# Kernel tuning notes

Measured on AMD Instinct MI355X. Metric: run time of the kernel, lower is better.

## Reference

```python
import jax, jax.numpy as jnp
import numpy as np

N_NODES = 100000
N_EDGES = 1600000
IN_DIM, HID_DIM, OUT_DIM = 256, 128, 64


def gcn_conv(x, row, col, w, W, b, n):
    # PyG GCNConv (eval): add self-loops (weight 1), symmetric normalization,
    # linear transform, scatter-add aggregation at target nodes.
    row = jnp.concatenate([row, jnp.arange(n, dtype=row.dtype)])
    col = jnp.concatenate([col, jnp.arange(n, dtype=col.dtype)])
    w = jnp.concatenate([w, jnp.ones((n,), dtype=w.dtype)])
    deg = jax.ops.segment_sum(w, col, num_segments=n)  # [N]
    dinv = jnp.where(deg > 0, jax.lax.rsqrt(deg), 0.0)
    norm = dinv[row] * w * dinv[col]  # [E+N]
    h = x @ W  # [N, out]
    msg = norm[:, None] * h[row]  # gather: [E+N, out]
    out = jax.ops.segment_sum(msg, col, num_segments=n)  # scatter-add
    return out + b


def setup_inputs() -> dict:
    key = jax.random.key(0)
    k = jax.random.split(key, 8)
    x = jax.random.normal(k[0], (N_NODES, IN_DIM), dtype=jnp.float32)
    edge_index = jax.random.randint(k[1], (2, N_EDGES), 0, N_NODES, dtype=jnp.int64)
    edge_weight = jax.random.uniform(k[2], (N_EDGES,), dtype=jnp.float32)
    s1 = 1.0 / np.sqrt(IN_DIM)
    s2 = 1.0 / np.sqrt(HID_DIM)
    W1 = jax.random.uniform(k[3], (IN_DIM, HID_DIM), minval=-s1, maxval=s1, dtype=jnp.float32)
    b1 = jnp.zeros((HID_DIM,), dtype=jnp.float32)
    W2 = jax.random.uniform(k[4], (HID_DIM, OUT_DIM), minval=-s2, maxval=s2, dtype=jnp.float32)
    b2 = jnp.zeros((OUT_DIM,), dtype=jnp.float32)
    return {"x": x, "edge_index": edge_index, "edge_weight": edge_weight,
            "W1": W1, "b1": b1, "W2": W2, "b2": b2}


def reference(x, edge_index, edge_weight, W1, b1, W2, b2):
    row, col = edge_index[0], edge_index[1]
    n = x.shape[0]
    h = gcn_conv(x, row, col, edge_weight, W1, b1, n)
    h = jax.nn.relu(h)  # dropout is identity in eval mode
    out = gcn_conv(h, row, col, edge_weight, W2, b2, n)
    return out
```

## Files before the change

### kernel.cpp

```cpp
#include <hip/hip_runtime.h>
#include <hip/hip_fp16.h>

#define IN_DIM 256
#define HID_DIM 128
#define OUT_DIM 64

typedef short s8v __attribute__((ext_vector_type(8)));
typedef float f32x4 __attribute__((ext_vector_type(4)));


__device__ __forceinline__ unsigned short bf16_rne(float f) {
    unsigned int u = __float_as_uint(f);
    u += 0x7FFFu + ((u >> 16) & 1u);
    return (unsigned short)(u >> 16);
}
__device__ __forceinline__ float bfbits_to_f(unsigned short h) {
    return __uint_as_float(((unsigned int)h) << 16);
}
__device__ __forceinline__ void cvt_split4(float4 f, uint2& hv, uint2& lv) {
    unsigned short h0 = bf16_rne(f.x), h1 = bf16_rne(f.y);
    unsigned short h2 = bf16_rne(f.z), h3 = bf16_rne(f.w);
    unsigned short l0 = bf16_rne(f.x - bfbits_to_f(h0));
    unsigned short l1 = bf16_rne(f.y - bfbits_to_f(h1));
    unsigned short l2 = bf16_rne(f.z - bfbits_to_f(h2));
    unsigned short l3 = bf16_rne(f.w - bfbits_to_f(h3));
    hv.x = (unsigned int)h0 | ((unsigned int)h1 << 16);
    hv.y = (unsigned int)h2 | ((unsigned int)h3 << 16);
    lv.x = (unsigned int)l0 | ((unsigned int)l1 << 16);
    lv.y = (unsigned int)l2 | ((unsigned int)l3 << 16);
}

__global__ __launch_bounds__(256) void wsplit_kernel(const float* __restrict__ W,
        unsigned short* __restrict__ wth, unsigned short* __restrict__ wtl,
        int K, int NCOL) {
    int idx = blockIdx.x * 256 + threadIdx.x;
    if (idx < K * NCOL) {
        int k = idx / NCOL, nn = idx % NCOL;
        float f = W[idx];
        unsigned short h = bf16_rne(f);
        unsigned short l = bf16_rne(f - bfbits_to_f(h));
        wth[nn * K + k] = h;
        wtl[nn * K + k] = l;
    }
}


#define FPSCALE 16777216.0f
#define FPMASK  ((1ULL << 40) - 1)

__global__ __launch_bounds__(256) void init_kernel(unsigned long long* packed, int n) {
    int i = blockIdx.x * 256 + threadIdx.x;
    if (i < n) packed[i] = (1ULL << 24);
}

__global__ __launch_bounds__(256) void deg_cnt_kernel(const int* __restrict__ col,
        const float* __restrict__ w, unsigned long long* packed,
        int* __restrict__ arr, int e) {
    int i = blockIdx.x * 256 + threadIdx.x;
    if (i < e) {
        unsigned long long v = (1ULL << 40) |
            (unsigned long long)(w[i] * FPSCALE + 0.5f);
        unsigned long long old = atomicAdd(&packed[col[i]], v);
        arr[i] = (int)(old >> 40);
    }
}

__global__ __launch_bounds__(256) void dinv_kernel(const unsigned long long* __restrict__ packed,
        float* __restrict__ dinv, int* __restrict__ cnt, int n) {
    int i = blockIdx.x * 256 + threadIdx.x;
    if (i < n) {
        unsigned long long p = packed[i];
        float d = (float)(p & FPMASK) * (1.0f / FPSCALE);
        dinv[i] = d > 0.0f ? rsqrtf(d) : 0.0f;
        cnt[i] = (int)(p >> 40);
    }
}


__global__ __launch_bounds__(256) void scan1_kernel(const int* __restrict__ cnt,
        int* __restrict__ bsum, int n) {
    int t = threadIdx.x;
    int base = blockIdx.x * 1024 + t * 4;
    int s = 0;
    if (base + 3 < n) {
        int4 v = *(const int4*)(cnt + base);
        s = v.x + v.y + v.z + v.w;
    } else {
        for (int i = 0; i < 4; i++) if (base + i < n) s += cnt[base + i];
    }
    __shared__ int sm[256];
    sm[t] = s;
    __syncthreads();
    for (int d = 1; d < 256; d <<= 1) {
        int v = (t >= d) ? sm[t - d] : 0;
        __syncthreads();
        sm[t] += v;
        __syncthreads();
    }
    if (t == 255) bsum[blockIdx.x] = sm[255];
}

__global__ __launch_bounds__(1024) void scan2_kernel(int* bsum, int* total_out, int nb) {
    __shared__ int sm[1024];
    int t = threadIdx.x;
    int v = (t < nb) ? bsum[t] : 0;
    sm[t] = v;
    __syncthreads();
    for (int d = 1; d < 1024; d <<= 1) {
        int u = (t >= d) ? sm[t - d] : 0;
        __syncthreads();
        sm[t] += u;
        __syncthreads();
    }
    int ex = (t == 0) ? 0 : sm[t - 1];
    if (t < nb) bsum[t] = ex;
    if (t == nb - 1) *total_out = sm[t];
}

__global__ __launch_bounds__(256) void scan3_kernel(const int* __restrict__ cnt,
        const int* __restrict__ bsum, int* __restrict__ offsets, int n) {
    int t = threadIdx.x;
    int base = blockIdx.x * 1024 + t * 4;
    int a[4] = {0, 0, 0, 0};
    if (base + 3 < n) {
        int4 v = *(const int4*)(cnt + base);
        a[0] = v.x; a[1] = v.y; a[2] = v.z; a[3] = v.w;
    } else {
        for (int i = 0; i < 4; i++) if (base + i < n) a[i] = cnt[base + i];
    }
    int s = a[0] + a[1] + a[2] + a[3];
    __shared__ int sm[256];
    sm[t] = s;
    __syncthreads();
    for (int d = 1; d < 256; d <<= 1) {
        int u = (t >= d) ? sm[t - d] : 0;
        __syncthreads();
        sm[t] += u;
        __syncthreads();
    }
    int pre = bsum[blockIdx.x] + ((t == 0) ? 0 : sm[t - 1]);
    int o0 = pre, o1 = o0 + a[0], o2 = o1 + a[1], o3 = o2 + a[2];
    if (base + 3 < n) {
        *(int4*)(offsets + base) = make_int4(o0, o1, o2, o3);
    } else {
        int o[4] = {o0, o1, o2, o3};
        for (int i = 0; i < 4; i++) if (base + i < n) offsets[base + i] = o[i];
    }
}


__global__ __launch_bounds__(256) void fill_csc_kernel(const int* __restrict__ row,
        const int* __restrict__ col, const float* __restrict__ w,
        const int* __restrict__ offsets, const int* __restrict__ arr,
        int2* __restrict__ csc, int e) {
    int i = blockIdx.x * 256 + threadIdx.x;
    if (i < e) {
        int c = col[i];
        int p = offsets[c] + arr[i];
        csc[p] = make_int2(row[i], __float_as_int(w[i]));
    }
}


template<int K, int NCOL>
__global__ __launch_bounds__(256) void gemm_mfma_kernel(
        const float* __restrict__ x, const unsigned short* __restrict__ wth,
        const unsigned short* __restrict__ wtl, const float* __restrict__ dinv,
        __half* __restrict__ out, int n) {
    constexpr int NT = NCOL / 16;
    constexpr int NCH = K / 32;
    __shared__ unsigned short sAh[128 * 40];
    __shared__ unsigned short sAl[128 * 40];
    __shared__ unsigned short sBh[NCOL * 40];
    __shared__ unsigned short sBl[NCOL * 40];

    int t = threadIdx.x;
    int wave = t >> 6, lane = t & 63, quad = lane >> 4, r16 = lane & 15;
    long rowBase = (long)blockIdx.x * 128;

    f32x4 acc[2][NT];
#pragma unroll
    for (int mi = 0; mi < 2; mi++)
#pragma unroll
        for (int nt = 0; nt < NT; nt++) acc[mi][nt] = (f32x4)0.0f;

    int srow = t >> 1;
    int skseg = (t & 1) * 16;
    long sgr = rowBase + srow; if (sgr > n - 1) sgr = n - 1;
    const float* xrow = x + sgr * K + skseg;

    for (int kc = 0; kc < NCH; kc++) {
        const float4* xs = (const float4*)(xrow + kc * 32);
        float4 f0 = xs[0], f1 = xs[1], f2 = xs[2], f3 = xs[3];
        uint2 h0, l0, h1, l1, h2, l2, h3, l3;
        cvt_split4(f0, h0, l0); cvt_split4(f1, h1, l1);
        cvt_split4(f2, h2, l2); cvt_split4(f3, h3, l3);
        *(uint4*)(sAh + srow * 40 + skseg)     = make_uint4(h0.x, h0.y, h1.x, h1.y);
        *(uint4*)(sAh + srow * 40 + skseg + 8) = make_uint4(h2.x, h2.y, h3.x, h3.y);
        *(uint4*)(sAl + srow * 40 + skseg)     = make_uint4(l0.x, l0.y, l1.x, l1.y);
        *(uint4*)(sAl + srow * 40 + skseg + 8) = make_uint4(l2.x, l2.y, l3.x, l3.y);
        for (int c = t; c < NCOL * 4; c += 256) {
            int nn = c >> 2, ks = (c & 3) * 8;
            *(uint4*)(sBh + nn * 40 + ks) = *(const uint4*)(wth + nn * K + kc * 32 + ks);
            *(uint4*)(sBl + nn * 40 + ks) = *(const uint4*)(wtl + nn * K + kc * 32 + ks);
        }
        __syncthreads();
        const unsigned short* pa  = sAh + (wave * 32 + r16) * 40 + quad * 8;
        const unsigned short* pal = sAl + (wave * 32 + r16) * 40 + quad * 8;
        s8v ah0 = *(const s8v*)pa;
        s8v ah1 = *(const s8v*)(pa + 16 * 40);
        s8v al0 = *(const s8v*)pal;
        s8v al1 = *(const s8v*)(pal + 16 * 40);
#pragma unroll
        for (int nt = 0; nt < NT; nt++) {
            const unsigned short* pb  = sBh + (nt * 16 + r16) * 40 + quad * 8;
            const unsigned short* pbl = sBl + (nt * 16 + r16) * 40 + quad * 8;
            s8v bh = *(const s8v*)pb;
            s8v bl = *(const s8v*)pbl;
            acc[0][nt] = __builtin_amdgcn_mfma_f32_16x16x32_bf16(ah0, bh, acc[0][nt], 0, 0, 0);
            acc[0][nt] = __builtin_amdgcn_mfma_f32_16x16x32_bf16(al0, bh, acc[0][nt], 0, 0, 0);
            acc[0][nt] = __builtin_amdgcn_mfma_f32_16x16x32_bf16(ah0, bl, acc[0][nt], 0, 0, 0);
            acc[1][nt] = __builtin_amdgcn_mfma_f32_16x16x32_bf16(ah1, bh, acc[1][nt], 0, 0, 0);
            acc[1][nt] = __builtin_amdgcn_mfma_f32_16x16x32_bf16(al1, bh, acc[1][nt], 0, 0, 0);
            acc[1][nt] = __builtin_amdgcn_mfma_f32_16x16x32_bf16(ah1, bl, acc[1][nt], 0, 0, 0);
        }
        __syncthreads();
    }
#pragma unroll
    for (int mi = 0; mi < 2; mi++) {
        long gr0 = rowBase + wave * 32 + mi * 16 + quad * 4;
#pragma unroll
        for (int nt = 0; nt < NT; nt++) {
            f32x4 d = acc[mi][nt];
#pragma unroll
            for (int i = 0; i < 4; i++) {
                long gr = gr0 + i;
                if (gr < n) out[gr * NCOL + nt * 16 + r16] =
                    __float2half(d[i] * dinv[gr]);
            }
        }
    }
}


__device__ __forceinline__ void acc8(float* a, uint4 raw, float w) {
    __half2* hp = (__half2*)&raw;
    float2 f0 = __half22float2(hp[0]);
    float2 f1 = __half22float2(hp[1]);
    float2 f2 = __half22float2(hp[2]);
    float2 f3 = __half22float2(hp[3]);
    a[0] += w * f0.x; a[1] += w * f0.y; a[2] += w * f1.x; a[3] += w * f1.y;
    a[4] += w * f2.x; a[5] += w * f2.y; a[6] += w * f3.x; a[7] += w * f3.y;
}

__device__ __forceinline__ void acc4h(float* a, uint2 raw, float w) {
    __half2* hp = (__half2*)&raw;
    float2 f0 = __half22float2(hp[0]);
    float2 f1 = __half22float2(hp[1]);
    a[0] += w * f0.x; a[1] += w * f0.y; a[2] += w * f1.x; a[3] += w * f1.y;
}


__global__ __launch_bounds__(256) void agg1_kernel(const __half* __restrict__ h,
        const float* __restrict__ dinv, const int* __restrict__ offsets,
        const int2* __restrict__ csc, const float* __restrict__ b,
        float* __restrict__ out, int n) {
    int t = threadIdx.x;
    int lane = t & 63;
    int strm = lane >> 4;
    int li = lane & 15;
    int node = blockIdx.x * 4 + (t >> 6);
    if (node >= n) return;

    float a0[8] = {0,0,0,0,0,0,0,0};
    float a1[8] = {0,0,0,0,0,0,0,0};
    int s = offsets[node], e = offsets[node + 1];

    if (strm == 0) {
        uint4 raw = ((const uint4*)(h + (long)node * HID_DIM))[li];
        acc8(a0, raw, 1.0f);
    }

    int p = s + strm;
    for (; p + 4 < e; p += 8) {
        int2 e0 = csc[p], e1 = csc[p + 4];
        uint4 r0 = ((const uint4*)(h + (long)e0.x * HID_DIM))[li];
        uint4 r1 = ((const uint4*)(h + (long)e1.x * HID_DIM))[li];
        acc8(a0, r0, __int_as_float(e0.y));
        acc8(a1, r1, __int_as_float(e1.y));
    }
    if (p < e) {
        int2 e0 = csc[p];
        uint4 r0 = ((const uint4*)(h + (long)e0.x * HID_DIM))[li];
        acc8(a0, r0, __int_as_float(e0.y));
    }
#pragma unroll
    for (int j = 0; j < 8; j++) a0[j] += a1[j];
#pragma unroll
    for (int j = 0; j < 8; j++) a0[j] += __shfl_down(a0[j], 32);
#pragma unroll
    for (int j = 0; j < 8; j++) a0[j] += __shfl_down(a0[j], 16);
    if (strm == 0) {
        float di = dinv[node];
        float4 bv0 = ((const float4*)b)[li * 2];
        float4 bv1 = ((const float4*)b)[li * 2 + 1];
        float4 o0 = make_float4(fmaxf(di * a0[0] + bv0.x, 0.f), fmaxf(di * a0[1] + bv0.y, 0.f),
                                fmaxf(di * a0[2] + bv0.z, 0.f), fmaxf(di * a0[3] + bv0.w, 0.f));
        float4 o1 = make_float4(fmaxf(di * a0[4] + bv1.x, 0.f), fmaxf(di * a0[5] + bv1.y, 0.f),
                                fmaxf(di * a0[6] + bv1.z, 0.f), fmaxf(di * a0[7] + bv1.w, 0.f));
        float4* dst = (float4*)(out + (long)node * HID_DIM);
        dst[li * 2] = o0;
        dst[li * 2 + 1] = o1;
    }
}


__global__ __launch_bounds__(256) void agg2_kernel(const __half* __restrict__ h,
        const float* __restrict__ dinv, const int* __restrict__ offsets,
        const int2* __restrict__ csc, const float* __restrict__ b,
        float* __restrict__ out, int n) {
    int t = threadIdx.x;
    int lane = t & 63;
    int strm = lane >> 4;
    int li = lane & 15;
    int node = blockIdx.x * 4 + (t >> 6);
    if (node >= n) return;

    float a0[4] = {0,0,0,0};
    float a1[4] = {0,0,0,0};
    int s = offsets[node], e = offsets[node + 1];

    if (strm == 0) {
        uint2 raw = ((const uint2*)(h + (long)node * OUT_DIM))[li];
        acc4h(a0, raw, 1.0f);
    }

    int p = s + strm;
    for (; p + 4 < e; p += 8) {
        int2 e0 = csc[p], e1 = csc[p + 4];
        uint2 r0 = ((const uint2*)(h + (long)e0.x * OUT_DIM))[li];
        uint2 r1 = ((const uint2*)(h + (long)e1.x * OUT_DIM))[li];
        acc4h(a0, r0, __int_as_float(e0.y));
        acc4h(a1, r1, __int_as_float(e1.y));
    }
    if (p < e) {
        int2 e0 = csc[p];
        uint2 r0 = ((const uint2*)(h + (long)e0.x * OUT_DIM))[li];
        acc4h(a0, r0, __int_as_float(e0.y));
    }
#pragma unroll
    for (int j = 0; j < 4; j++) a0[j] += a1[j];
#pragma unroll
    for (int j = 0; j < 4; j++) a0[j] += __shfl_down(a0[j], 32);
#pragma unroll
    for (int j = 0; j < 4; j++) a0[j] += __shfl_down(a0[j], 16);
    if (strm == 0) {
        float di = dinv[node];
        float4 bv = ((const float4*)b)[li];
        ((float4*)(out + (long)node * OUT_DIM))[li] =
            make_float4(di * a0[0] + bv.x, di * a0[1] + bv.y,
                        di * a0[2] + bv.z, di * a0[3] + bv.w);
    }
}


extern "C" void kernel_launch(void* const* d_in, const int* in_sizes, int n_in,
                              void* d_out, int out_size, void* d_ws, size_t ws_size,
                              hipStream_t stream) {
    const float* x  = (const float*)d_in[0];
    const int*   ei = (const int*)d_in[1];
    const float* w  = (const float*)d_in[2];
    const float* W1 = (const float*)d_in[3];
    const float* b1 = (const float*)d_in[4];
    const float* W2 = (const float*)d_in[5];
    const float* b2 = (const float*)d_in[6];
    float* out = (float*)d_out;

    int N = in_sizes[0] / IN_DIM;
    int E = in_sizes[2];
    const int* row = ei;
    const int* col = ei + E;

    char* base = (char*)d_ws;
    size_t off = 0;
    auto alloc = [&](size_t bytes) -> void* {
        void* p = base + off;
        off += (bytes + 255) & ~(size_t)255;
        return p;
    };
    unsigned long long* packed = (unsigned long long*)alloc((size_t)N * 8);
    float* dinv     = (float*)alloc((size_t)N * 4);
    int*   cnt      = (int*)  alloc((size_t)N * 4);
    int*   offsets  = (int*)  alloc((size_t)(N + 1) * 4);
    int*   arr      = (int*)  alloc((size_t)E * 4);
    int*   bsum     = (int*)  alloc((size_t)1024 * 4);
    int2*  csc      = (int2*) alloc((size_t)E * 8);
    __half* h       = (__half*)alloc((size_t)N * HID_DIM * 2);
    float* hagg     = (float*)alloc((size_t)N * HID_DIM * 4);
    unsigned short* wt1h = (unsigned short*)alloc((size_t)IN_DIM * HID_DIM * 2);
    unsigned short* wt1l = (unsigned short*)alloc((size_t)IN_DIM * HID_DIM * 2);
    unsigned short* wt2h = (unsigned short*)alloc((size_t)HID_DIM * OUT_DIM * 2);
    unsigned short* wt2l = (unsigned short*)alloc((size_t)HID_DIM * OUT_DIM * 2);

    int gN = (N + 255) / 256;
    int gE = (E + 255) / 256;
    int gGemm = (N + 127) / 128;
    int gAgg = (N + 3) / 4;
    int nbScan = (N + 1023) / 1024;

    wsplit_kernel<<<(IN_DIM * HID_DIM + 255) / 256, 256, 0, stream>>>(
        W1, wt1h, wt1l, IN_DIM, HID_DIM);
    wsplit_kernel<<<(HID_DIM * OUT_DIM + 255) / 256, 256, 0, stream>>>(
        W2, wt2h, wt2l, HID_DIM, OUT_DIM);
    init_kernel<<<gN, 256, 0, stream>>>(packed, N);
    deg_cnt_kernel<<<gE, 256, 0, stream>>>(col, w, packed, arr, E);
    dinv_kernel<<<gN, 256, 0, stream>>>(packed, dinv, cnt, N);
    scan1_kernel<<<nbScan, 256, 0, stream>>>(cnt, bsum, N);
    scan2_kernel<<<1, 1024, 0, stream>>>(bsum, offsets + N, nbScan);
    scan3_kernel<<<nbScan, 256, 0, stream>>>(cnt, bsum, offsets, N);
    fill_csc_kernel<<<gE, 256, 0, stream>>>(row, col, w, offsets, arr, csc, E);
    gemm_mfma_kernel<IN_DIM, HID_DIM><<<gGemm, 256, 0, stream>>>(x, wt1h, wt1l, dinv, h, N);
    agg1_kernel<<<gAgg, 256, 0, stream>>>(h, dinv, offsets, csc, b1, hagg, N);
    gemm_mfma_kernel<HID_DIM, OUT_DIM><<<gGemm, 256, 0, stream>>>(hagg, wt2h, wt2l, dinv, h, N);
    agg2_kernel<<<gAgg, 256, 0, stream>>>(h, dinv, offsets, csc, b2, out, N);
}
```

Measured before the change: 475.8 us.

## Load GEMM operands directly into MFMA registers, drop LDS staging and barriers

The MFMA GEMM kernel stops staging the A (x) and B (split weights) tiles in shared memory. Each lane now loads its MFMA fragment straight from global memory, and the A loads for the next K chunk are prefetched into registers while the current chunk computes. Both __syncthreads per chunk go away. In exchange, every wave re-reads the B fragments from global/L2 and the A row accesses are less coalesced, so the saved LDS traffic and synchronisation may be offset by extra global load traffic.

Result: slower. 517.6 us (+8.8%).

```diff
diff --git a/kernel.cpp b/kernel.cpp
--- a/kernel.cpp
+++ b/kernel.cpp
@@ -30,6 +30,16 @@
     lv.y = (unsigned int)l2 | ((unsigned int)l3 << 16);
 }
 
+__device__ __forceinline__ void cvt_split8(float4 f0, float4 f1, s8v& hi, s8v& lo) {
+    uint2 h0, l0, h1, l1;
+    cvt_split4(f0, h0, l0);
+    cvt_split4(f1, h1, l1);
+    uint4 h = make_uint4(h0.x, h0.y, h1.x, h1.y);
+    uint4 l = make_uint4(l0.x, l0.y, l1.x, l1.y);
+    hi = *(s8v*)&h;
+    lo = *(s8v*)&l;
+}
+
 __global__ __launch_bounds__(256) void wsplit_kernel(const float* __restrict__ W,
         unsigned short* __restrict__ wth, unsigned short* __restrict__ wtl,
         int K, int NCOL) {
@@ -169,10 +179,6 @@
         __half* __restrict__ out, int n) {
     constexpr int NT = NCOL / 16;
     constexpr int NCH = K / 32;
-    __shared__ unsigned short sAh[128 * 40];
-    __shared__ unsigned short sAl[128 * 40];
-    __shared__ unsigned short sBh[NCOL * 40];
-    __shared__ unsigned short sBl[NCOL * 40];
 
     int t = threadIdx.x;
     int wave = t >> 6, lane = t & 63, quad = lane >> 4, r16 = lane & 15;
@@ -184,39 +190,36 @@
 #pragma unroll
         for (int nt = 0; nt < NT; nt++) acc[mi][nt] = (f32x4)0.0f;
 
-    int srow = t >> 1;
-    int skseg = (t & 1) * 16;
-    long sgr = rowBase + srow; if (sgr > n - 1) sgr = n - 1;
-    const float* xrow = x + sgr * K + skseg;
+    long r0 = rowBase + wave * 32 + r16;       if (r0 > n - 1) r0 = n - 1;
+    long r1 = rowBase + wave * 32 + 16 + r16;  if (r1 > n - 1) r1 = n - 1;
+    const float* pa0 = x + r0 * K + quad * 8;
+    const float* pa1 = x + r1 * K + quad * 8;
+    const unsigned short* pbh = wth + (long)r16 * K + quad * 8;
+    const unsigned short* pbl = wtl + (long)r16 * K + quad * 8;
+
+    float4 a0 = *(const float4*)(pa0);
+    float4 a1 = *(const float4*)(pa0 + 4);
+    float4 a2 = *(const float4*)(pa1);
+    float4 a3 = *(const float4*)(pa1 + 4);
 
     for (int kc = 0; kc < NCH; kc++) {
-        const float4* xs = (const float4*)(xrow + kc * 32);
-        float4 f0 = xs[0], f1 = xs[1], f2 = xs[2], f3 = xs[3];
-        uint2 h0, l0, h1, l1, h2, l2, h3, l3;
-        cvt_split4(f0, h0, l0); cvt_split4(f1, h1, l1);
-        cvt_split4(f2, h2, l2); cvt_split4(f3, h3, l3);
-        *(uint4*)(sAh + srow * 40 + skseg)     = make_uint4(h0.x, h0.y, h1.x, h1.y);
-        *(uint4*)(sAh + srow * 40 + skseg + 8) = make_uint4(h2.x, h2.y, h3.x, h3.y);
-        *(uint4*)(sAl + srow * 40 + skseg)     = make_uint4(l0.x, l0.y, l1.x, l1.y);
-        *(uint4*)(sAl + srow * 40 + skseg + 8) = make_uint4(l2.x, l2.y, l3.x, l3.y);
-        for (int c = t; c < NCOL * 4; c += 256) {
-            int nn = c >> 2, ks = (c & 3) * 8;
-            *(uint4*)(sBh + nn * 40 + ks) = *(const uint4*)(wth + nn * K + kc * 32 + ks);
-            *(uint4*)(sBl + nn * 40 + ks) = *(const uint4*)(wtl + nn * K + kc * 32 + ks);
+        s8v ah0, al0, ah1, al1;
+        cvt_split8(a0, a1, ah0, al0);
+        cvt_split8(a2, a3, ah1, al1);
+        if (kc + 1 < NCH) {
+            const float* q0 = pa0 + (kc + 1) * 32;
+            const float* q1 = pa1 + (kc + 1) * 32;
+            a0 = *(const float4*)(q0);
+            a1 = *(const float4*)(q0 + 4);
+            a2 = *(const float4*)(q1);
+            a3 = *(const float4*)(q1 + 4);
         }
-        __syncthreads();
-        const unsigned short* pa  = sAh + (wave * 32 + r16) * 40 + quad * 8;
-        const unsigned short* pal = sAl + (wave * 32 + r16) * 40 + quad * 8;
-        s8v ah0 = *(const s8v*)pa;
-        s8v ah1 = *(const s8v*)(pa + 16 * 40);
-        s8v al0 = *(const s8v*)pal;
-        s8v al1 = *(const s8v*)(pal + 16 * 40);
+        const unsigned short* bkh = pbh + kc * 32;
+        const unsigned short* bkl = pbl + kc * 32;
 #pragma unroll
         for (int nt = 0; nt < NT; nt++) {
-            const unsigned short* pb  = sBh + (nt * 16 + r16) * 40 + quad * 8;
-            const unsigned short* pbl = sBl + (nt * 16 + r16) * 40 + quad * 8;
-            s8v bh = *(const s8v*)pb;
-            s8v bl = *(const s8v*)pbl;
+            s8v bh = *(const s8v*)(bkh + nt * 16 * K);
+            s8v bl = *(const s8v*)(bkl + nt * 16 * K);
             acc[0][nt] = __builtin_amdgcn_mfma_f32_16x16x32_bf16(ah0, bh, acc[0][nt], 0, 0, 0);
             acc[0][nt] = __builtin_amdgcn_mfma_f32_16x16x32_bf16(al0, bh, acc[0][nt], 0, 0, 0);
             acc[0][nt] = __builtin_amdgcn_mfma_f32_16x16x32_bf16(ah0, bl, acc[0][nt], 0, 0, 0);
@@ -224,7 +227,6 @@
             acc[1][nt] = __builtin_amdgcn_mfma_f32_16x16x32_bf16(al1, bh, acc[1][nt], 0, 0, 0);
             acc[1][nt] = __builtin_amdgcn_mfma_f32_16x16x32_bf16(ah1, bl, acc[1][nt], 0, 0, 0);
         }
-        __syncthreads();
     }
 #pragma unroll
     for (int mi = 0; mi < 2; mi++) {
```
